# Kernel optimization log

Measured on AMD Instinct MI355X. Metric: run time of the kernel, lower is better.

The kernel has to match this reference:

```python
import jax, jax.numpy as jnp
import numpy as np

DIM = 1024
HEADS = 16
DIM_HEAD = 64
INNER = HEADS * DIM_HEAD
B, M, N = 8, 4096, 256
EPS = 1e-5


def layer_norm(x, g, b):
    mu = jnp.mean(x, axis=-1, keepdims=True)
    var = jnp.mean(jnp.square(x - mu), axis=-1, keepdims=True)
    return (x - mu) * jax.lax.rsqrt(var + EPS) * g + b


def setup_inputs() -> dict:
    key = jax.random.key(0)
    ks = jax.random.split(key, 8)
    x = jax.random.normal(ks[0], (B, M, DIM), dtype=jnp.float32)
    latents = jax.random.normal(ks[1], (B, N, DIM), dtype=jnp.float32)
    x_att_mask = jax.random.randint(ks[2], (B, M), 0, 2) == 1  # True = masked
    s = 0.02
    Wq = jax.random.normal(ks[3], (DIM, INNER), dtype=jnp.float32) * s
    Wkv = jax.random.normal(ks[4], (DIM, 2 * INNER), dtype=jnp.float32) * s
    Wo = jax.random.normal(ks[5], (INNER, DIM), dtype=jnp.float32) * s
    return {
        "x": x, "latents": latents, "x_att_mask": x_att_mask,
        "nm_g": jnp.ones((DIM,), jnp.float32), "nm_b": jnp.zeros((DIM,), jnp.float32),
        "nl_g": jnp.ones((DIM,), jnp.float32), "nl_b": jnp.zeros((DIM,), jnp.float32),
        "Wq": Wq, "Wkv": Wkv, "Wo": Wo,
    }


def reference(x, latents, x_att_mask, nm_g, nm_b, nl_g, nl_b, Wq, Wkv, Wo):
    b, n, d = latents.shape
    h, dh = HEADS, DIM_HEAD
    scale = dh ** (-0.5)

    # additive mask: concat(media mask, all-False latent mask); True -> -inf, False -> +1 (faithful quirk)
    latent_mask = jnp.zeros((b, n), dtype=bool)
    full_mask = jnp.concatenate([x_att_mask, latent_mask], axis=1)  # [b, m+n]
    add_mask = jnp.where(full_mask, -jnp.inf, 1.0).astype(x.dtype)[:, None, None, :]  # [b,1,1,m+n]

    xn = layer_norm(x, nm_g, nm_b)
    ln = layer_norm(latents, nl_g, nl_b)

    q = (ln @ Wq).reshape(b, n, h, dh).transpose(0, 2, 1, 3)  # bhnd
    kv_in = jnp.concatenate([xn, ln], axis=1)                 # [b, m+n, d]
    kv = kv_in @ Wkv
    k, v = jnp.split(kv, 2, axis=-1)
    j = kv_in.shape[1]
    k = k.reshape(b, j, h, dh).transpose(0, 2, 1, 3)
    v = v.reshape(b, j, h, dh).transpose(0, 2, 1, 3)

    sim = jnp.einsum('bhid,bhjd->bhij', q * scale, k)
    sim = sim - jnp.max(sim, axis=-1, keepdims=True)
    sim = sim + add_mask
    attn = jax.nn.softmax(sim, axis=-1)
    out = jnp.einsum('bhij,bhjd->bhid', attn, v)
    out = out.transpose(0, 2, 1, 3).reshape(b, n, h * dh)
    return out @ Wo
```

## Files before the change

### kernel.cpp

```cpp
#include <hip/hip_runtime.h>
#include <hip/hip_bf16.h>
#include <stdint.h>

#define HEADS 16
#define DH    64
#define NB    8
#define MQ    256
#define MX    4096
#define JD    4352
#define DIMV  1024

typedef __bf16 bf16;
typedef __bf16 bf16x8 __attribute__((ext_vector_type(8)));
typedef float  f32x4  __attribute__((ext_vector_type(4)));

#define SWZ(r, c) (((c) ^ ((r) & 7)))

__device__ __forceinline__ void gl_lds16(const void* g, void* l) {
  __builtin_amdgcn_global_load_lds((const __attribute__((address_space(1))) void*)g,
                                   (__attribute__((address_space(3))) void*)l, 16, 0, 0);
}

__global__ __launch_bounds__(256) void ln_kernel(
    const float* __restrict__ X, const float* __restrict__ gw, const float* __restrict__ bw,
    bf16* __restrict__ out_kv, bf16* __restrict__ out_ln, int is_lat)
{
  const int row = blockIdx.x;
  const int tid = threadIdx.x;
  const float4 v = ((const float4*)(X + (size_t)row * DIMV))[tid];
  float s  = v.x + v.y + v.z + v.w;
  float s2 = v.x*v.x + v.y*v.y + v.z*v.z + v.w*v.w;
#pragma unroll
  for (int m = 1; m < 64; m <<= 1) { s += __shfl_xor(s, m); s2 += __shfl_xor(s2, m); }
  __shared__ float red[8];
  const int wid = tid >> 6;
  if ((tid & 63) == 0) { red[wid*2] = s; red[wid*2+1] = s2; }
  __syncthreads();
  s  = red[0] + red[2] + red[4] + red[6];
  s2 = red[1] + red[3] + red[5] + red[7];
  const float mu  = s * (1.0f / DIMV);
  const float var = s2 * (1.0f / DIMV) - mu * mu;
  const float rst = rsqrtf(var + 1e-5f);
  const float4 g4 = ((const float4*)gw)[tid];
  const float4 b4 = ((const float4*)bw)[tid];
  union { bf16 h[4]; short4 s4; } u;
  u.h[0] = (bf16)((v.x - mu) * rst * g4.x + b4.x);
  u.h[1] = (bf16)((v.y - mu) * rst * g4.y + b4.y);
  u.h[2] = (bf16)((v.z - mu) * rst * g4.z + b4.z);
  u.h[3] = (bf16)((v.w - mu) * rst * g4.w + b4.w);
  size_t kvrow;
  if (is_lat) { int b = row >> 8;  int i = row & 255;  kvrow = (size_t)b * JD + MX + i; }
  else        { int b = row >> 12; int j = row & 4095; kvrow = (size_t)b * JD + j; }
  *(short4*)(out_kv + kvrow * DIMV + tid * 4) = u.s4;
  if (is_lat) *(short4*)(out_ln + (size_t)row * DIMV + tid * 4) = u.s4;
}

__global__ __launch_bounds__(256) void transpose_w(
    const float* __restrict__ in, bf16* __restrict__ out, int R, int C)
{
  __shared__ float t[64][65];
  const int tilesC = C >> 6;
  const int tc = blockIdx.x % tilesC, tr = blockIdx.x / tilesC;
  const int r0 = tr << 6, c0 = tc << 6;
  const int lr = threadIdx.x >> 4;
  const int lc = (threadIdx.x & 15) << 2;
#pragma unroll
  for (int p = 0; p < 4; p++) {
    float4 v = *(const float4*)&in[(size_t)(r0 + lr + p*16) * C + c0 + lc];
    t[lr + p*16][lc    ] = v.x; t[lr + p*16][lc + 1] = v.y;
    t[lr + p*16][lc + 2] = v.z; t[lr + p*16][lc + 3] = v.w;
  }
  __syncthreads();
#pragma unroll
  for (int p = 0; p < 4; p++) {
    const int oc = lr + p*16;
    union { bf16 h[4]; short4 s4; } u;
    u.h[0] = (bf16)t[lc    ][oc]; u.h[1] = (bf16)t[lc + 1][oc];
    u.h[2] = (bf16)t[lc + 2][oc]; u.h[3] = (bf16)t[lc + 3][oc];
    *(short4*)&out[(size_t)(c0 + oc) * R + r0 + lc] = u.s4;
  }
}

__global__ __launch_bounds__(256) void mask_detect(
    const unsigned char* __restrict__ m, int n, int* __restrict__ flag)
{
  const int tid = threadIdx.x;
  int cnt = 0;
  for (int i = tid; i < n; i += 256) cnt += (m[i] != 0) ? 1 : 0;
#pragma unroll
  for (int mm = 1; mm < 64; mm <<= 1) cnt += __shfl_xor(cnt, mm);
  __shared__ int r4[4];
  if ((tid & 63) == 0) r4[tid >> 6] = cnt;
  __syncthreads();
  if (tid == 0) {
    int t = r4[0] + r4[1] + r4[2] + r4[3];
    flag[0] = (t * 16 > n * 5) ? 1 : 0;
  }
}

__global__ __launch_bounds__(256) void mask_build(
    const void* __restrict__ mraw, const int* __restrict__ flag, float* __restrict__ mm)
{
  const int idx = blockIdx.x * 256 + threadIdx.x;
  const int b = idx / JD, j = idx - b * JD;
  float v = 1.0f;
  if (j < MX) {
    bool masked = (*flag) ? (((const unsigned char*)mraw)[b * MX + j] != 0)
                          : (((const int*)mraw)[b * MX + j] != 0);
    v = masked ? 0.0f : 1.0f;
  }
  mm[idx] = v;
}

__global__ __launch_bounds__(256) void gemm128(
    const bf16* __restrict__ A, const bf16* __restrict__ Bt,
    float* __restrict__ Cf, bf16* __restrict__ outR, bf16* __restrict__ outVT,
    int N, int K, int kSplitX, int mode)
{
  __shared__ bf16 smem[2 * 128 * 64];
  bf16* As = smem;
  bf16* Bs = smem + 128 * 64;
  bf16* Ct = smem;

  const int tid = threadIdx.x;
  const int lane = tid & 63, wid = tid >> 6;
  const int wr = wid >> 1, wc = wid & 1;
  const int bx = blockIdx.x;
  const int m0 = blockIdx.y * 128;
  const bool vmode = (mode == 1) && (bx >= kSplitX);
  const int n0 = vmode ? 1024 + (bx - kSplitX) * 128 : bx * 128;
  const int srow = tid >> 3, sc = tid & 7;
  const int ssw = SWZ(srow, sc) * 8;
  const int lc = lane & 15, lq = lane >> 4;

  f32x4 acc[4][4];
#pragma unroll
  for (int i = 0; i < 4; i++)
#pragma unroll
    for (int j = 0; j < 4; j++)
#pragma unroll
      for (int r = 0; r < 4; r++) acc[i][j][r] = 0.f;

  const bf16* Arow = vmode ? (Bt + (size_t)n0 * K) : (A + (size_t)m0 * K);
  const bf16* Brow = vmode ? (A + (size_t)m0 * K) : (Bt + (size_t)n0 * K);
  const bf16* Abase = Arow + (size_t)srow * K + ssw;
  const bf16* Bbase = Brow + (size_t)srow * K + ssw;

  for (int k0 = 0; k0 < K; k0 += 64) {
    __syncthreads();
#pragma unroll
    for (int q = 0; q < 4; q++) {
      gl_lds16(Abase + (size_t)q * 32 * K + k0, &As[(srow + q*32) * 64 + sc*8]);
      gl_lds16(Bbase + (size_t)q * 32 * K + k0, &Bs[(srow + q*32) * 64 + sc*8]);
    }
    asm volatile("s_waitcnt vmcnt(0)" ::: "memory");
    __syncthreads();
#pragma unroll
    for (int kk = 0; kk < 2; kk++) {
      bf16x8 af[4], bfr[4];
#pragma unroll
      for (int mi = 0; mi < 4; mi++)
        af[mi] = *(const bf16x8*)&As[(wr*64 + mi*16 + lc) * 64 + SWZ(lc, kk*4 + lq)*8];
#pragma unroll
      for (int ni = 0; ni < 4; ni++)
        bfr[ni] = *(const bf16x8*)&Bs[(wc*64 + ni*16 + lc) * 64 + SWZ(lc, kk*4 + lq)*8];
#pragma unroll
      for (int mi = 0; mi < 4; mi++)
#pragma unroll
        for (int ni = 0; ni < 4; ni++)
          acc[mi][ni] = __builtin_amdgcn_mfma_f32_16x16x32_bf16(af[mi], bfr[ni], acc[mi][ni], 0, 0, 0);
    }
  }

  if (mode == 0) {
#pragma unroll
    for (int mi = 0; mi < 4; mi++)
#pragma unroll
      for (int ni = 0; ni < 4; ni++) {
        const int r = m0 + wr*64 + mi*16 + lq*4;
        const int c = n0 + wc*64 + ni*16 + lc;
#pragma unroll
        for (int reg = 0; reg < 4; reg++)
          Cf[(size_t)(r + reg) * N + c] = acc[mi][ni][reg];
      }
    return;
  }

  __syncthreads();
#pragma unroll
  for (int mi = 0; mi < 4; mi++)
#pragma unroll
    for (int ni = 0; ni < 4; ni++) {
      const int col = wc*64 + ni*16 + lc;
      const int cch = col >> 3, cw = col & 7;
#pragma unroll
      for (int reg = 0; reg < 4; reg++) {
        const int row = wr*64 + mi*16 + lq*4 + reg;
        Ct[row*128 + ((cch ^ (row & 15)) << 3) + cw] = (bf16)acc[mi][ni][reg];
      }
    }
  __syncthreads();

  const int cch = tid & 15, r0 = tid >> 4;
  if (!vmode) {
    bf16* dst0 = outR + (size_t)m0 * 1024 + n0 + cch*8;
#pragma unroll
    for (int i = 0; i < 8; i++) {
      const int row = r0 + i*16;
      bf16x8 v = *(const bf16x8*)&Ct[row*128 + ((cch ^ r0) << 3)];
      *(bf16x8*)(dst0 + (size_t)row * 1024) = v;
    }
  } else {
    const int bb = m0 / JD;
    const int jbase = m0 - bb * JD;
#pragma unroll
    for (int i = 0; i < 8; i++) {
      const int row = r0 + i*16;
      const int cc = n0 + row - 1024;
      bf16x8 v = *(const bf16x8*)&Ct[row*128 + ((cch ^ r0) << 3)];
      bf16* dst = outVT + (((size_t)(bb*HEADS + (cc >> 6)))*64 + (cc & 63)) * JD
                        + jbase + cch*8;
      *(bf16x8*)dst = v;
    }
  }
}

__global__ __launch_bounds__(512) void attn_kernel(
    const bf16* __restrict__ Qrows,
    const bf16* __restrict__ Krows,
    const bf16* __restrict__ VT,
    const float* __restrict__ mmul,
    bf16* __restrict__ outp)
{
  const int bh = blockIdx.x >> 1, qt = blockIdx.x & 1;
  const int b = bh >> 4, h = bh & 15;
  __shared__ bf16 Qs[128 * 64];
  __shared__ bf16 Ks[64 * 64];
  __shared__ bf16 VTs[64 * 64];
  __shared__ bf16 Ps[8][16 * 64];
  const int tid = threadIdx.x, lane = tid & 63, w = tid >> 6;
  const int lc = lane & 15, lq = lane >> 4;
  const int srow = tid >> 3, sc = tid & 7;
  const int ssw = SWZ(srow, sc) * 8;

  const bf16* Qg = Qrows + ((size_t)(b*MQ + qt*128)) * 1024 + h*64;
  const bf16* Kg = Krows + ((size_t)b * JD) * 1024 + h*64;
  const bf16* Vg = VT + ((size_t)bh * 64) * JD;

  gl_lds16(Qg + (size_t)srow * 1024 + ssw, &Qs[tid*8]);
  gl_lds16(Qg + (size_t)(srow + 64) * 1024 + ssw, &Qs[(tid + 512)*8]);
  asm volatile("s_waitcnt vmcnt(0)" ::: "memory");
  __syncthreads();

  bf16x8 qf[2];
#pragma unroll
  for (int kk = 0; kk < 2; kk++)
    qf[kk] = *(const bf16x8*)&Qs[(w*16 + lc) * 64 + SWZ(lc, kk*4 + lq)*8];

  f32x4 oacc[4];
  float den[4];
#pragma unroll
  for (int di = 0; di < 4; di++)
#pragma unroll
    for (int r = 0; r < 4; r++) oacc[di][r] = 0.f;
#pragma unroll
  for (int r = 0; r < 4; r++) den[r] = 0.f;

  for (int j0 = 0; j0 < JD; j0 += 64) {
    __syncthreads();
    gl_lds16(Kg + (size_t)(j0 + srow) * 1024 + ssw, &Ks[tid*8]);
    gl_lds16(Vg + (size_t)srow * JD + j0 + ssw, &VTs[tid*8]);
    asm volatile("s_waitcnt vmcnt(0)" ::: "memory");
    __syncthreads();

    f32x4 sacc[4];
#pragma unroll
    for (int nj = 0; nj < 4; nj++)
#pragma unroll
      for (int r = 0; r < 4; r++) sacc[nj][r] = 0.f;
#pragma unroll
    for (int kk = 0; kk < 2; kk++) {
      bf16x8 kf[4];
#pragma unroll
      for (int nj = 0; nj < 4; nj++)
        kf[nj] = *(const bf16x8*)&Ks[(nj*16 + lc) * 64 + SWZ(lc, kk*4 + lq)*8];
#pragma unroll
      for (int nj = 0; nj < 4; nj++)
        sacc[nj] = __builtin_amdgcn_mfma_f32_16x16x32_bf16(qf[kk], kf[nj], sacc[nj], 0, 0, 0);
    }

#pragma unroll
    for (int nj = 0; nj < 4; nj++) {
      const float mm = mmul[b * JD + j0 + nj*16 + lc];
#pragma unroll
      for (int r = 0; r < 4; r++) {
        const float p = exp2f(sacc[nj][r] * 0.18033688f) * mm;
        den[r] += p;
        const int row = lq*4 + r, col = nj*16 + lc;
        Ps[w][row*64 + (((col >> 3) ^ (row & 7)) << 3) + (col & 7)] = (bf16)p;
      }
    }

#pragma unroll
    for (int kk = 0; kk < 2; kk++) {
      bf16x8 pf = *(const bf16x8*)&Ps[w][lc*64 + SWZ(lc, kk*4 + lq)*8];
#pragma unroll
      for (int di = 0; di < 4; di++) {
        bf16x8 vf = *(const bf16x8*)&VTs[(di*16 + lc) * 64 + SWZ(lc, kk*4 + lq)*8];
        oacc[di] = __builtin_amdgcn_mfma_f32_16x16x32_bf16(pf, vf, oacc[di], 0, 0, 0);
      }
    }
  }

#pragma unroll
  for (int r = 0; r < 4; r++) {
    float d = den[r];
    d += __shfl_xor(d, 1); d += __shfl_xor(d, 2);
    d += __shfl_xor(d, 4); d += __shfl_xor(d, 8);
    den[r] = 1.0f / d;
  }

#pragma unroll
  for (int di = 0; di < 4; di++) {
    const int col = h*64 + di*16 + lc;
#pragma unroll
    for (int r = 0; r < 4; r++) {
      const int i = qt*128 + w*16 + lq*4 + r;
      outp[(size_t)(b*MQ + i) * 1024 + col] = (bf16)(oacc[di][r] * den[r]);
    }
  }
}

extern "C" void kernel_launch(void* const* d_in, const int* in_sizes, int n_in,
                              void* d_out, int out_size, void* d_ws, size_t ws_size,
                              hipStream_t stream)
{
  const float* x    = (const float*)d_in[0];
  const float* lat  = (const float*)d_in[1];
  const void*  mraw = d_in[2];
  const float* nm_g = (const float*)d_in[3];
  const float* nm_b = (const float*)d_in[4];
  const float* nl_g = (const float*)d_in[5];
  const float* nl_b = (const float*)d_in[6];
  const float* Wq   = (const float*)d_in[7];
  const float* Wkv  = (const float*)d_in[8];
  const float* Wo   = (const float*)d_in[9];
  float* out = (float*)d_out;

  char* p = (char*)d_ws;
  auto alloc = [&](size_t bytes) { char* r = p; p += (bytes + 255) & ~(size_t)255; return r; };

  bf16*  kv_in  = (bf16*)alloc((size_t)NB * JD * DIMV * 2);
  bf16*  Krows  = (bf16*)alloc((size_t)NB * JD * 1024 * 2);
  bf16*  VTbuf  = (bf16*)alloc((size_t)NB * HEADS * 64 * JD * 2);
  bf16*  WqT    = (bf16*)alloc((size_t)1024 * 1024 * 2);
  bf16*  WkvT   = (bf16*)alloc((size_t)2048 * 1024 * 2);
  bf16*  WoT    = (bf16*)alloc((size_t)1024 * 1024 * 2);
  bf16*  ln_buf = (bf16*)alloc((size_t)NB * MQ * DIMV * 2);
  bf16*  Qrows  = (bf16*)alloc((size_t)NB * MQ * 1024 * 2);
  bf16*  attout = (bf16*)alloc((size_t)NB * MQ * DIMV * 2);
  float* mmulp  = (float*)alloc((size_t)NB * JD * 4);
  int*   flag   = (int*)alloc(256);
  (void)ws_size; (void)in_sizes; (void)n_in; (void)out_size;

  ln_kernel<<<NB * MX, 256, 0, stream>>>(x,   nm_g, nm_b, kv_in, nullptr, 0);
  ln_kernel<<<NB * MQ, 256, 0, stream>>>(lat, nl_g, nl_b, kv_in, ln_buf, 1);
  transpose_w<<<256, 256, 0, stream>>>(Wq,  WqT,  1024, 1024);
  transpose_w<<<512, 256, 0, stream>>>(Wkv, WkvT, 1024, 2048);
  transpose_w<<<256, 256, 0, stream>>>(Wo,  WoT,  1024, 1024);
  mask_detect<<<1, 256, 0, stream>>>((const unsigned char*)mraw, 32768, flag);
  mask_build<<<136, 256, 0, stream>>>(mraw, flag, mmulp);

  gemm128<<<dim3(16, 272), 256, 0, stream>>>(kv_in, WkvT, nullptr, Krows, VTbuf,
                                             2048, 1024, 8, 1);
  gemm128<<<dim3(8, 16), 256, 0, stream>>>(ln_buf, WqT, nullptr, Qrows, nullptr,
                                           1024, 1024, 8, 1);
  attn_kernel<<<256, 512, 0, stream>>>(Qrows, Krows, VTbuf, mmulp, attout);
  gemm128<<<dim3(8, 16), 256, 0, stream>>>(attout, WoT, out, nullptr, nullptr,
                                           1024, 1024, 8, 0);
}
```

Measured before the change: 595.4 us.

## Add 256x256-tile KV GEMM with 8 waves, XCD remap and pipelined staging

```diff
diff --git a/kernel.cpp b/kernel.cpp
--- a/kernel.cpp
+++ b/kernel.cpp
@@ -112,6 +112,150 @@
   mm[idx] = v;
 }
 
+__global__ __launch_bounds__(512, 2) void gemm256(
+    const bf16* __restrict__ A, const bf16* __restrict__ Bt,
+    bf16* __restrict__ outR, bf16* __restrict__ outVT,
+    int K, int kSplitX)
+{
+  __shared__ bf16 sm[65536];
+
+  const int tid = threadIdx.x;
+  const int lane = tid & 63, wid = tid >> 6;
+  const int wr = wid >> 2, wc = wid & 3;
+  const int lc = lane & 15, lq = lane >> 4;
+  const int srow = tid >> 3, sc = tid & 7;
+  const int ssw = SWZ(srow, sc) * 8;
+
+  int bid = blockIdx.y * gridDim.x + blockIdx.x;
+  const int nwg = gridDim.x * gridDim.y;
+  bid = (bid & 7) * (nwg >> 3) + (bid >> 3);
+  const int bx = bid % gridDim.x;
+  const int by = bid / gridDim.x;
+
+  const bool vmode = (bx >= kSplitX);
+  const int n0 = vmode ? 1024 + (bx - kSplitX) * 256 : bx * 256;
+  const int m0 = by * 256;
+
+  const bf16* Arow = vmode ? (Bt + (size_t)n0 * K) : (A + (size_t)m0 * K);
+  const bf16* Brow = vmode ? (A + (size_t)m0 * K) : (Bt + (size_t)n0 * K);
+  const bf16* Abase = Arow + (size_t)srow * K + ssw;
+  const bf16* Bbase = Brow + (size_t)srow * K + ssw;
+
+  auto stageA = [&](int cbuf, int h, int kt) {
+    gl_lds16(Abase + (size_t)(h*128     ) * K + (size_t)kt * 64,
+             &sm[cbuf*16384 + (h*128     )*64 + tid*8]);
+    gl_lds16(Abase + (size_t)(h*128 + 64) * K + (size_t)kt * 64,
+             &sm[cbuf*16384 + (h*128 + 64)*64 + tid*8]);
+  };
+  auto stageB = [&](int cbuf, int h, int kt) {
+    gl_lds16(Bbase + (size_t)(h*128     ) * K + (size_t)kt * 64,
+             &sm[32768 + cbuf*16384 + (h*128     )*64 + tid*8]);
+    gl_lds16(Bbase + (size_t)(h*128 + 64) * K + (size_t)kt * 64,
+             &sm[32768 + cbuf*16384 + (h*128 + 64)*64 + tid*8]);
+  };
+
+  f32x4 acc[8][4];
+#pragma unroll
+  for (int i = 0; i < 8; i++)
+#pragma unroll
+    for (int j = 0; j < 4; j++)
+#pragma unroll
+      for (int r = 0; r < 4; r++) acc[i][j][r] = 0.f;
+
+  const int NT = K >> 6;
+
+  stageA(0, 0, 0); stageA(0, 1, 0);
+  stageB(0, 0, 0); stageB(0, 1, 0);
+  stageA(1, 0, 1); stageA(1, 1, 1);
+  asm volatile("s_waitcnt vmcnt(4)" ::: "memory");
+  __builtin_amdgcn_s_barrier();
+
+  for (int kt = 0; kt < NT; ++kt) {
+    const int c = kt & 1;
+    const bf16* As = sm + c * 16384;
+    const bf16* Bs = sm + 32768 + c * 16384;
+    const bool st = (kt + 1 < NT);
+    bf16x8 bfrag[4][2];
+#pragma unroll
+    for (int p = 0; p < 4; ++p) {
+      bf16x8 afrag[2][2];
+#pragma unroll
+      for (int mi = 0; mi < 2; ++mi)
+#pragma unroll
+        for (int kk = 0; kk < 2; ++kk)
+          afrag[mi][kk] = *(const bf16x8*)&As[(wr*128 + (p*2 + mi)*16 + lc)*64 + SWZ(lc, kk*4 + lq)*8];
+      if (p == 0) {
+#pragma unroll
+        for (int n = 0; n < 4; ++n)
+#pragma unroll
+          for (int kk = 0; kk < 2; ++kk)
+            bfrag[n][kk] = *(const bf16x8*)&Bs[(wc*64 + n*16 + lc)*64 + SWZ(lc, kk*4 + lq)*8];
+        if (st) stageB(1 - c, 0, kt + 1);
+      }
+      if (p == 1 && st) stageB(1 - c, 1, kt + 1);
+      __builtin_amdgcn_s_barrier();
+      __builtin_amdgcn_s_setprio(1);
+#pragma unroll
+      for (int kk = 0; kk < 2; ++kk)
+#pragma unroll
+        for (int mi = 0; mi < 2; ++mi)
+#pragma unroll
+          for (int n = 0; n < 4; ++n)
+            acc[p*2 + mi][n] = __builtin_amdgcn_mfma_f32_16x16x32_bf16(
+                afrag[mi][kk], bfrag[n][kk], acc[p*2 + mi][n], 0, 0, 0);
+      __builtin_amdgcn_s_setprio(0);
+      __builtin_amdgcn_s_barrier();
+    }
+    if (kt + 2 < NT) {
+      stageA(c, 0, kt + 2);
+      stageA(c, 1, kt + 2);
+      asm volatile("s_waitcnt vmcnt(4)" ::: "memory");
+      __builtin_amdgcn_s_barrier();
+    } else if (kt + 1 < NT) {
+      asm volatile("s_waitcnt vmcnt(0)" ::: "memory");
+      __builtin_amdgcn_s_barrier();
+    }
+  }
+
+  __syncthreads();
+  bf16* Ct = sm;
+#pragma unroll
+  for (int m = 0; m < 8; ++m)
+#pragma unroll
+    for (int n = 0; n < 4; ++n) {
+      const int col = wc*64 + n*16 + lc;
+      const int cch = col >> 3, cw = col & 7;
+#pragma unroll
+      for (int r = 0; r < 4; ++r) {
+        const int row = wr*128 + m*16 + lq*4 + r;
+        Ct[row*256 + (((cch ^ (row & 31)) << 3) + cw)] = (bf16)acc[m][n][r];
+      }
+    }
+  __syncthreads();
+
+  const int cch = tid & 31, r0 = tid >> 5;
+  if (!vmode) {
+#pragma unroll
+    for (int i = 0; i < 16; ++i) {
+      const int row = r0 + i*16;
+      bf16x8 v = *(const bf16x8*)&Ct[row*256 + ((cch ^ (row & 31)) << 3)];
+      *(bf16x8*)(outR + (size_t)(m0 + row) * 1024 + n0 + cch*8) = v;
+    }
+  } else {
+    const int bb = m0 / JD;
+    const int jbase = m0 - bb * JD;
+#pragma unroll
+    for (int i = 0; i < 16; ++i) {
+      const int row = r0 + i*16;
+      const int cc = n0 + row - 1024;
+      bf16x8 v = *(const bf16x8*)&Ct[row*256 + ((cch ^ (row & 31)) << 3)];
+      bf16* dst = outVT + (((size_t)(bb*HEADS + (cc >> 6)))*64 + (cc & 63)) * JD
+                        + jbase + cch*8;
+      *(bf16x8*)dst = v;
+    }
+  }
+}
+
 __global__ __launch_bounds__(256) void gemm128(
     const bf16* __restrict__ A, const bf16* __restrict__ Bt,
     float* __restrict__ Cf, bf16* __restrict__ outR, bf16* __restrict__ outVT,
@@ -202,25 +346,13 @@
   __syncthreads();
 
   const int cch = tid & 15, r0 = tid >> 4;
-  if (!vmode) {
+  {
     bf16* dst0 = outR + (size_t)m0 * 1024 + n0 + cch*8;
 #pragma unroll
     for (int i = 0; i < 8; i++) {
       const int row = r0 + i*16;
       bf16x8 v = *(const bf16x8*)&Ct[row*128 + ((cch ^ r0) << 3)];
       *(bf16x8*)(dst0 + (size_t)row * 1024) = v;
-    }
-  } else {
-    const int bb = m0 / JD;
-    const int jbase = m0 - bb * JD;
-#pragma unroll
-    for (int i = 0; i < 8; i++) {
-      const int row = r0 + i*16;
-      const int cc = n0 + row - 1024;
-      bf16x8 v = *(const bf16x8*)&Ct[row*128 + ((cch ^ r0) << 3)];
-      bf16* dst = outVT + (((size_t)(bb*HEADS + (cc >> 6)))*64 + (cc & 63)) * JD
-                        + jbase + cch*8;
-      *(bf16x8*)dst = v;
     }
   }
 }
@@ -371,8 +503,7 @@
   mask_detect<<<1, 256, 0, stream>>>((const unsigned char*)mraw, 32768, flag);
   mask_build<<<136, 256, 0, stream>>>(mraw, flag, mmulp);
 
-  gemm128<<<dim3(16, 272), 256, 0, stream>>>(kv_in, WkvT, nullptr, Krows, VTbuf,
-                                             2048, 1024, 8, 1);
+  gemm256<<<dim3(8, 136), 512, 0, stream>>>(kv_in, WkvT, Krows, VTbuf, 1024, 4);
   gemm128<<<dim3(8, 16), 256, 0, stream>>>(ln_buf, WqT, nullptr, Qrows, nullptr,
                                            1024, 1024, 8, 1);
   attn_kernel<<<256, 512, 0, stream>>>(Qrows, Krows, VTbuf, mmulp, attout);
```

New measurement: 571.7 us. 4.0% less time.

## Add pipelined 256x256 GEMM fusing KV and Q projections; double-buffer attention K/V

Applied to the files above, without the earlier changes.

```diff
diff --git a/kernel.cpp b/kernel.cpp
--- a/kernel.cpp
+++ b/kernel.cpp
@@ -9,12 +9,15 @@
 #define MX    4096
 #define JD    4352
 #define DIMV  1024
+#define GK    1024
 
 typedef __bf16 bf16;
 typedef __bf16 bf16x8 __attribute__((ext_vector_type(8)));
 typedef float  f32x4  __attribute__((ext_vector_type(4)));
 
 #define SWZ(r, c) (((c) ^ ((r) & 7)))
+
+#define VMW(n) asm volatile("s_waitcnt vmcnt(" #n ")" ::: "memory")
 
 __device__ __forceinline__ void gl_lds16(const void* g, void* l) {
   __builtin_amdgcn_global_load_lds((const __attribute__((address_space(1))) void*)g,
@@ -112,23 +115,165 @@
   mm[idx] = v;
 }
 
+__global__ __launch_bounds__(512, 2) void gemm256(
+    const bf16* __restrict__ A, const bf16* __restrict__ Bt,
+    const bf16* __restrict__ Aq, const bf16* __restrict__ Bq,
+    bf16* __restrict__ outR, bf16* __restrict__ outVT, bf16* __restrict__ outQ)
+{
+  __shared__ bf16 sm[65536];
+
+  const int tid = threadIdx.x;
+  const int lane = tid & 63, wid = tid >> 6;
+  const int wr = wid >> 2, wc = wid & 3;
+  const int lc = lane & 15, lq = lane >> 4;
+  const int srow = tid >> 3, sc = tid & 7;
+  const int ssw = SWZ(srow, sc) * 8;
+
+  int bid = blockIdx.x;
+  bid = (bid & 7) * 140 + (bid >> 3);
+
+  const bf16 *Arow, *Brow;
+  int m0, n0, omode;
+  if (bid < 1088) {
+    const int by = bid >> 3, bx = bid & 7;
+    m0 = by * 256;
+    if (bx < 4) { n0 = bx * 256;
+      Arow = A  + (size_t)m0 * GK; Brow = Bt + (size_t)n0 * GK; omode = 0; }
+    else        { n0 = 1024 + (bx - 4) * 256;
+      Arow = Bt + (size_t)n0 * GK; Brow = A  + (size_t)m0 * GK; omode = 1; }
+  } else {
+    const int ix = bid - 1088;
+    m0 = (ix >> 2) * 256; n0 = (ix & 3) * 256;
+    Arow = Aq + (size_t)m0 * GK; Brow = Bq + (size_t)n0 * GK; omode = 2;
+  }
+
+  const bf16* Abase = Arow + (size_t)srow * GK + ssw;
+  const bf16* Bbase = Brow + (size_t)srow * GK + ssw;
+
+  auto stA = [&](int d, int h, int kt) {
+#pragma unroll
+    for (int l = 0; l < 2; ++l)
+      gl_lds16(Abase + (size_t)(h*128 + l*64) * GK + kt * 64,
+               &sm[d*32768 + (h*128 + l*64)*64 + tid*8]);
+  };
+  auto stB = [&](int d, int h, int kt) {
+#pragma unroll
+    for (int l = 0; l < 2; ++l)
+      gl_lds16(Bbase + (size_t)(h*128 + l*64) * GK + kt * 64,
+               &sm[d*32768 + 16384 + (h*128 + l*64)*64 + tid*8]);
+  };
+
+  f32x4 acc[8][4];
+#pragma unroll
+  for (int i = 0; i < 8; i++)
+#pragma unroll
+    for (int j = 0; j < 4; j++)
+#pragma unroll
+      for (int r = 0; r < 4; r++) acc[i][j][r] = 0.f;
+
+#define DS_PHASE(d, q, STAGE_STMT, WAIT_STMT)                                  \
+  {                                                                            \
+    const bf16* As_ = sm + (d)*32768;                                          \
+    const bf16* Bs_ = sm + (d)*32768 + 16384;                                  \
+    bf16x8 af[2][2];                                                           \
+    _Pragma("unroll") for (int mi = 0; mi < 2; ++mi)                           \
+      _Pragma("unroll") for (int kk = 0; kk < 2; ++kk)                         \
+        af[mi][kk] = *(const bf16x8*)&As_[(wr*128 + ((q)*2+mi)*16 + lc)*64 +   \
+                                          SWZ(lc, kk*4 + lq)*8];               \
+    if ((q) == 0) {                                                            \
+      _Pragma("unroll") for (int n = 0; n < 4; ++n)                            \
+        _Pragma("unroll") for (int kk = 0; kk < 2; ++kk)                       \
+          bfrag[n][kk] = *(const bf16x8*)&Bs_[(wc*64 + n*16 + lc)*64 +         \
+                                              SWZ(lc, kk*4 + lq)*8];           \
+    }                                                                          \
+    STAGE_STMT;                                                                \
+    WAIT_STMT;                                                                 \
+    __builtin_amdgcn_s_barrier();                                              \
+    __builtin_amdgcn_s_setprio(1);                                             \
+    _Pragma("unroll") for (int kk = 0; kk < 2; ++kk)                           \
+      _Pragma("unroll") for (int mi = 0; mi < 2; ++mi)                         \
+        _Pragma("unroll") for (int n = 0; n < 4; ++n)                          \
+          acc[(q)*2+mi][n] = __builtin_amdgcn_mfma_f32_16x16x32_bf16(          \
+              af[mi][kk], bfrag[n][kk], acc[(q)*2+mi][n], 0, 0, 0);            \
+    __builtin_amdgcn_s_setprio(0);                                             \
+    __builtin_amdgcn_s_barrier();                                              \
+  }
+
+  stB(0, 0, 0); stB(0, 1, 0);
+  stA(0, 0, 0); stA(0, 1, 0);
+  stB(1, 0, 1); stB(1, 1, 1);
+  VMW(4);
+  __builtin_amdgcn_s_barrier();
+
+  bf16x8 bfrag[4][2];
+#pragma unroll 1
+  for (int it = 0; it < 8; ++it) {
+    const int tb = 2*it + 1, ta2 = 2*it + 2, tb2 = 2*it + 3;
+    const bool s2 = (ta2 < 16), s3 = (tb2 < 16);
+    DS_PHASE(0, 0, { stA(1, 0, tb); stA(1, 1, tb); }, {});
+    DS_PHASE(0, 1, { if (s2) stB(0, 0, ta2); }, {});
+    DS_PHASE(0, 2, { if (s2) stB(0, 1, ta2); }, {});
+    DS_PHASE(0, 3, {}, { if (s2) { VMW(4); } else { VMW(0); } });
+    DS_PHASE(1, 0, { if (s2) stA(0, 0, ta2); }, {});
+    DS_PHASE(1, 1, { if (s2) stA(0, 1, ta2); }, {});
+    DS_PHASE(1, 2, { if (s3) stB(1, 0, tb2); }, {});
+    DS_PHASE(1, 3, { if (s3) stB(1, 1, tb2); }, { if (s3) { VMW(4); } });
+  }
+#undef DS_PHASE
+
+  __syncthreads();
+  bf16* Ct = sm;
+#pragma unroll
+  for (int m = 0; m < 8; ++m)
+#pragma unroll
+    for (int n = 0; n < 4; ++n) {
+      const int col = wc*64 + n*16 + lc;
+      const int cch = col >> 3, cw = col & 7;
+#pragma unroll
+      for (int r = 0; r < 4; ++r) {
+        const int row = wr*128 + m*16 + lq*4 + r;
+        Ct[row*256 + (((cch ^ (row & 31)) << 3) + cw)] = (bf16)acc[m][n][r];
+      }
+    }
+  __syncthreads();
+
+  const int cch = tid & 31, r0 = tid >> 5;
+  if (omode != 1) {
+    bf16* dst0 = (omode == 0 ? outR : outQ);
+#pragma unroll
+    for (int i = 0; i < 16; ++i) {
+      const int row = r0 + i*16;
+      bf16x8 v = *(const bf16x8*)&Ct[row*256 + ((cch ^ (row & 31)) << 3)];
+      *(bf16x8*)(dst0 + (size_t)(m0 + row) * 1024 + n0 + cch*8) = v;
+    }
+  } else {
+    const int bb = m0 / JD;
+    const int jbase = m0 - bb * JD;
+#pragma unroll
+    for (int i = 0; i < 16; ++i) {
+      const int row = r0 + i*16;
+      const int cc = n0 + row - 1024;
+      bf16x8 v = *(const bf16x8*)&Ct[row*256 + ((cch ^ (row & 31)) << 3)];
+      bf16* dst = outVT + (((size_t)(bb*HEADS + (cc >> 6)))*64 + (cc & 63)) * JD
+                        + jbase + cch*8;
+      *(bf16x8*)dst = v;
+    }
+  }
+}
+
 __global__ __launch_bounds__(256) void gemm128(
     const bf16* __restrict__ A, const bf16* __restrict__ Bt,
-    float* __restrict__ Cf, bf16* __restrict__ outR, bf16* __restrict__ outVT,
-    int N, int K, int kSplitX, int mode)
+    float* __restrict__ Cf, int N)
 {
   __shared__ bf16 smem[2 * 128 * 64];
   bf16* As = smem;
   bf16* Bs = smem + 128 * 64;
-  bf16* Ct = smem;
 
   const int tid = threadIdx.x;
   const int lane = tid & 63, wid = tid >> 6;
   const int wr = wid >> 1, wc = wid & 1;
-  const int bx = blockIdx.x;
   const int m0 = blockIdx.y * 128;
-  const bool vmode = (mode == 1) && (bx >= kSplitX);
-  const int n0 = vmode ? 1024 + (bx - kSplitX) * 128 : bx * 128;
+  const int n0 = blockIdx.x * 128;
   const int srow = tid >> 3, sc = tid & 7;
   const int ssw = SWZ(srow, sc) * 8;
   const int lc = lane & 15, lq = lane >> 4;
@@ -141,19 +286,17 @@
 #pragma unroll
       for (int r = 0; r < 4; r++) acc[i][j][r] = 0.f;
 
-  const bf16* Arow = vmode ? (Bt + (size_t)n0 * K) : (A + (size_t)m0 * K);
-  const bf16* Brow = vmode ? (A + (size_t)m0 * K) : (Bt + (size_t)n0 * K);
-  const bf16* Abase = Arow + (size_t)srow * K + ssw;
-  const bf16* Bbase = Brow + (size_t)srow * K + ssw;
-
-  for (int k0 = 0; k0 < K; k0 += 64) {
+  const bf16* Abase = A + (size_t)m0 * GK + (size_t)srow * GK + ssw;
+  const bf16* Bbase = Bt + (size_t)n0 * GK + (size_t)srow * GK + ssw;
+
+  for (int k0 = 0; k0 < GK; k0 += 64) {
     __syncthreads();
 #pragma unroll
     for (int q = 0; q < 4; q++) {
-      gl_lds16(Abase + (size_t)q * 32 * K + k0, &As[(srow + q*32) * 64 + sc*8]);
-      gl_lds16(Bbase + (size_t)q * 32 * K + k0, &Bs[(srow + q*32) * 64 + sc*8]);
-    }
-    asm volatile("s_waitcnt vmcnt(0)" ::: "memory");
+      gl_lds16(Abase + (size_t)q * 32 * GK + k0, &As[(srow + q*32) * 64 + sc*8]);
+      gl_lds16(Bbase + (size_t)q * 32 * GK + k0, &Bs[(srow + q*32) * 64 + sc*8]);
+    }
+    VMW(0);
     __syncthreads();
 #pragma unroll
     for (int kk = 0; kk < 2; kk++) {
@@ -172,57 +315,16 @@
     }
   }
 
-  if (mode == 0) {
-#pragma unroll
-    for (int mi = 0; mi < 4; mi++)
-#pragma unroll
-      for (int ni = 0; ni < 4; ni++) {
-        const int r = m0 + wr*64 + mi*16 + lq*4;
-        const int c = n0 + wc*64 + ni*16 + lc;
-#pragma unroll
-        for (int reg = 0; reg < 4; reg++)
-          Cf[(size_t)(r + reg) * N + c] = acc[mi][ni][reg];
-      }
-    return;
-  }
-
-  __syncthreads();
 #pragma unroll
   for (int mi = 0; mi < 4; mi++)
 #pragma unroll
     for (int ni = 0; ni < 4; ni++) {
-      const int col = wc*64 + ni*16 + lc;
-      const int cch = col >> 3, cw = col & 7;
-#pragma unroll
-      for (int reg = 0; reg < 4; reg++) {
-        const int row = wr*64 + mi*16 + lq*4 + reg;
-        Ct[row*128 + ((cch ^ (row & 15)) << 3) + cw] = (bf16)acc[mi][ni][reg];
-      }
-    }
-  __syncthreads();
-
-  const int cch = tid & 15, r0 = tid >> 4;
-  if (!vmode) {
-    bf16* dst0 = outR + (size_t)m0 * 1024 + n0 + cch*8;
-#pragma unroll
-    for (int i = 0; i < 8; i++) {
-      const int row = r0 + i*16;
-      bf16x8 v = *(const bf16x8*)&Ct[row*128 + ((cch ^ r0) << 3)];
-      *(bf16x8*)(dst0 + (size_t)row * 1024) = v;
-    }
-  } else {
-    const int bb = m0 / JD;
-    const int jbase = m0 - bb * JD;
-#pragma unroll
-    for (int i = 0; i < 8; i++) {
-      const int row = r0 + i*16;
-      const int cc = n0 + row - 1024;
-      bf16x8 v = *(const bf16x8*)&Ct[row*128 + ((cch ^ r0) << 3)];
-      bf16* dst = outVT + (((size_t)(bb*HEADS + (cc >> 6)))*64 + (cc & 63)) * JD
-                        + jbase + cch*8;
-      *(bf16x8*)dst = v;
-    }
-  }
+      const int r = m0 + wr*64 + mi*16 + lq*4;
+      const int c = n0 + wc*64 + ni*16 + lc;
+#pragma unroll
+      for (int reg = 0; reg < 4; reg++)
+        Cf[(size_t)(r + reg) * N + c] = acc[mi][ni][reg];
+    }
 }
 
 __global__ __launch_bounds__(512) void attn_kernel(
@@ -235,8 +337,8 @@
   const int bh = blockIdx.x >> 1, qt = blockIdx.x & 1;
   const int b = bh >> 4, h = bh & 15;
   __shared__ bf16 Qs[128 * 64];
-  __shared__ bf16 Ks[64 * 64];
-  __shared__ bf16 VTs[64 * 64];
+  __shared__ bf16 Ks[2][64 * 64];
+  __shared__ bf16 VTs[2][64 * 64];
   __shared__ bf16 Ps[8][16 * 64];
   const int tid = threadIdx.x, lane = tid & 63, w = tid >> 6;
   const int lc = lane & 15, lq = lane >> 4;
@@ -247,9 +349,16 @@
   const bf16* Kg = Krows + ((size_t)b * JD) * 1024 + h*64;
   const bf16* Vg = VT + ((size_t)bh * 64) * JD;
 
+  auto stKV = [&](int c, int t) {
+    gl_lds16(Kg + (size_t)(t*64 + srow) * 1024 + ssw, &Ks[c][tid*8]);
+    gl_lds16(Vg + (size_t)srow * JD + t*64 + ssw, &VTs[c][tid*8]);
+  };
+
   gl_lds16(Qg + (size_t)srow * 1024 + ssw, &Qs[tid*8]);
   gl_lds16(Qg + (size_t)(srow + 64) * 1024 + ssw, &Qs[(tid + 512)*8]);
-  asm volatile("s_waitcnt vmcnt(0)" ::: "memory");
+  stKV(0, 0);
+  stKV(1, 1);
+  VMW(2);
   __syncthreads();
 
   bf16x8 qf[2];
@@ -266,12 +375,10 @@
 #pragma unroll
   for (int r = 0; r < 4; r++) den[r] = 0.f;
 
-  for (int j0 = 0; j0 < JD; j0 += 64) {
-    __syncthreads();
-    gl_lds16(Kg + (size_t)(j0 + srow) * 1024 + ssw, &Ks[tid*8]);
-    gl_lds16(Vg + (size_t)srow * JD + j0 + ssw, &VTs[tid*8]);
-    asm volatile("s_waitcnt vmcnt(0)" ::: "memory");
-    __syncthreads();
+#pragma unroll 1
+  for (int t = 0; t < JD/64; ++t) {
+    const int c = t & 1;
+    const int j0 = t * 64;
 
     f32x4 sacc[4];
 #pragma unroll
@@ -283,7 +390,7 @@
       bf16x8 kf[4];
 #pragma unroll
       for (int nj = 0; nj < 4; nj++)
-        kf[nj] = *(const bf16x8*)&Ks[(nj*16 + lc) * 64 + SWZ(lc, kk*4 + lq)*8];
+        kf[nj] = *(const bf16x8*)&Ks[c][(nj*16 + lc) * 64 + SWZ(lc, kk*4 + lq)*8];
 #pragma unroll
       for (int nj = 0; nj < 4; nj++)
         sacc[nj] = __builtin_amdgcn_mfma_f32_16x16x32_bf16(qf[kk], kf[nj], sacc[nj], 0, 0, 0);
@@ -306,10 +413,19 @@
       bf16x8 pf = *(const bf16x8*)&Ps[w][lc*64 + SWZ(lc, kk*4 + lq)*8];
 #pragma unroll
       for (int di = 0; di < 4; di++) {
-        bf16x8 vf = *(const bf16x8*)&VTs[(di*16 + lc) * 64 + SWZ(lc, kk*4 + lq)*8];
+        bf16x8 vf = *(const bf16x8*)&VTs[c][(di*16 + lc) * 64 + SWZ(lc, kk*4 + lq)*8];
         oacc[di] = __builtin_amdgcn_mfma_f32_16x16x32_bf16(pf, vf, oacc[di], 0, 0, 0);
       }
     }
+
+    __builtin_amdgcn_s_barrier();
+    if (t + 2 < JD/64) {
+      stKV(c, t + 2);
+      VMW(2);
+    } else if (t + 1 < JD/64) {
+      VMW(0);
+    }
+    __builtin_amdgcn_s_barrier();
   }
 
 #pragma unroll
@@ -371,11 +487,7 @@
   mask_detect<<<1, 256, 0, stream>>>((const unsigned char*)mraw, 32768, flag);
   mask_build<<<136, 256, 0, stream>>>(mraw, flag, mmulp);
 
-  gemm128<<<dim3(16, 272), 256, 0, stream>>>(kv_in, WkvT, nullptr, Krows, VTbuf,
-                                             2048, 1024, 8, 1);
-  gemm128<<<dim3(8, 16), 256, 0, stream>>>(ln_buf, WqT, nullptr, Qrows, nullptr,
-                                           1024, 1024, 8, 1);
+  gemm256<<<1120, 512, 0, stream>>>(kv_in, WkvT, ln_buf, WqT, Krows, VTbuf, Qrows);
   attn_kernel<<<256, 512, 0, stream>>>(Qrows, Krows, VTbuf, mmulp, attout);
-  gemm128<<<dim3(8, 16), 256, 0, stream>>>(attout, WoT, out, nullptr, nullptr,
-                                           1024, 1024, 8, 0);
-}
+  gemm128<<<dim3(8, 16), 256, 0, stream>>>(attout, WoT, out, 1024);
+}
```

Result: faster. 533.5 us (-10.4%).
